# Kernel optimization log

Measured on AMD Instinct MI355X. Metric: run time of the kernel, lower is better.

## Reference

```python
import jax, jax.numpy as jnp
import numpy as np

N_HEADS = 16
EPS = 1e-12  # torch F.normalize eps


def srmsnorm(x):
    # F.normalize(x, dim=-1) * sqrt(dim)
    d = x.shape[-1]
    norm = jnp.sqrt(jnp.sum(x * x, axis=-1, keepdims=True))
    return x / jnp.maximum(norm, EPS) * jnp.sqrt(jnp.float32(d))


def setup_inputs() -> dict:
    key = jax.random.key(0)
    ks = jax.random.split(key, 7)
    B, S, D, F = 2, 2048, 1024, 4096
    x = jax.random.normal(ks[0], (B, S, D), dtype=jnp.float32)
    # xavier-uniform-ish scale for square weights
    lim = np.sqrt(6.0 / (D + D)).astype(np.float32)
    wq = jax.random.uniform(ks[1], (D, D), jnp.float32, -lim, lim)
    wk = jax.random.uniform(ks[2], (D, D), jnp.float32, -lim, lim)
    wv = jax.random.uniform(ks[3], (D, D), jnp.float32, -lim, lim)
    wo = jax.random.uniform(ks[4], (D, D), jnp.float32, -lim, lim)
    w_in = jax.random.normal(ks[5], (D, F), dtype=jnp.float32) * np.sqrt(2.0 / D).astype(np.float32)
    lim2 = np.sqrt(6.0 / (D + F)).astype(np.float32)
    w_out = jax.random.uniform(ks[6], (F, D), jnp.float32, -lim2, lim2)
    return {"x": x, "wq": wq, "wk": wk, "wv": wv, "wo": wo, "w_in": w_in, "w_out": w_out}


def attention(x, wq, wk, wv, wo):
    B, S, D = x.shape
    H = N_HEADS
    hd = D // H
    scale = hd ** -0.5
    q = (x @ wq).reshape(B, S, H, hd).transpose(0, 2, 1, 3)  # [B,H,S,hd]
    k = (x @ wk).reshape(B, S, H, hd).transpose(0, 2, 1, 3)
    v = (x @ wv).reshape(B, S, H, hd).transpose(0, 2, 1, 3)
    scores = jnp.einsum('bhqd,bhkd->bhqk', q, k) * scale  # [B,H,S,S]
    causal = jnp.tril(jnp.ones((S, S), dtype=bool))
    scores = jnp.where(causal, scores, jnp.float32(-jnp.inf))
    probs = jax.nn.softmax(scores, axis=-1)
    out = jnp.einsum('bhqk,bhkd->bhqd', probs, v)  # [B,H,S,hd]
    out = out.transpose(0, 2, 1, 3).reshape(B, S, D)
    return out @ wo


def reference(x, wq, wk, wv, wo, w_in, w_out):
    h = x + attention(srmsnorm(x), wq, wk, wv, wo)
    ff = jax.nn.gelu(srmsnorm(h) @ w_in, approximate=True) @ w_out
    return h + ff
```

## Files before the change

kernel.cpp:

```cpp
#include <hip/hip_runtime.h>
#include <math.h>

#define BB 2
#define SS 2048
#define DD 1024
#define FF 4096
#define HH 16
#define MM (BB * SS)

typedef __attribute__((ext_vector_type(8))) short short8v;
typedef __attribute__((ext_vector_type(4))) float float4v;
typedef __attribute__((ext_vector_type(4))) unsigned short ushort4v;
typedef __attribute__((ext_vector_type(8))) unsigned short ushort8v;
typedef unsigned short u16;
typedef unsigned int u32;

#define MFMA16(A_, B_, C_) __builtin_amdgcn_mfma_f32_16x16x32_bf16((A_), (B_), (C_), 0, 0, 0)

__device__ __forceinline__ u16 f2bf(float f) {
    u32 u = __float_as_uint(f);
    u += 0x7FFF + ((u >> 16) & 1);
    return (u16)(u >> 16);
}

__device__ __forceinline__ void async16(void* lds, const void* g) {
    __builtin_amdgcn_global_load_lds(
        (const __attribute__((address_space(1))) u32*)g,
        (__attribute__((address_space(3))) u32*)lds, 16, 0, 0);
}

__device__ __forceinline__ float gelu_f(float x) {
    float u = 0.7978845608028654f * x * (1.0f + 0.044715f * x * x);
    float e = exp2f(u * 2.8853900817779268f);
    float th = 1.0f - 2.0f / (e + 1.0f);
    return 0.5f * x * (1.0f + th);
}

__global__ __launch_bounds__(256) void srmsnorm_bf16(const float* __restrict__ in,
                                                     u16* __restrict__ out) {
    const int row = blockIdx.x, t = threadIdx.x;
    float4 a = reinterpret_cast<const float4*>(in + (size_t)row * DD)[t];
    float ss = a.x * a.x + a.y * a.y + a.z * a.z + a.w * a.w;
#pragma unroll
    for (int off = 32; off > 0; off >>= 1) ss += __shfl_xor(ss, off);
    __shared__ float red[4];
    if ((t & 63) == 0) red[t >> 6] = ss;
    __syncthreads();
    float tot = red[0] + red[1] + red[2] + red[3];
    float sc = 32.0f / fmaxf(sqrtf(tot), 1e-12f);
    ushort4v ov;
    ov[0] = f2bf(a.x * sc); ov[1] = f2bf(a.y * sc);
    ov[2] = f2bf(a.z * sc); ov[3] = f2bf(a.w * sc);
    *(ushort4v*)(out + (size_t)row * DD + t * 4) = ov;
}

__global__ __launch_bounds__(256) void wtrans(const float* __restrict__ in,
                                              u16* __restrict__ out, int K, int N) {
    __shared__ float T[64][65];
    const int t = threadIdx.x;
    const int n0 = blockIdx.x * 64, k0 = blockIdx.y * 64;
#pragma unroll
    for (int i = 0; i < 4; ++i) {
        int r = i * 16 + (t >> 4), c4 = (t & 15) * 4;
        float4 v = *reinterpret_cast<const float4*>(in + (size_t)(k0 + r) * N + n0 + c4);
        T[r][c4 + 0] = v.x; T[r][c4 + 1] = v.y; T[r][c4 + 2] = v.z; T[r][c4 + 3] = v.w;
    }
    __syncthreads();
#pragma unroll
    for (int i = 0; i < 4; ++i) {
        int r = i * 16 + (t >> 4), c4 = (t & 15) * 4;
        ushort4v ov;
#pragma unroll
        for (int j = 0; j < 4; ++j) ov[j] = f2bf(T[c4 + j][r]);
        *(ushort4v*)(out + (size_t)(n0 + r) * K + k0 + c4) = ov;
    }
}

__global__ __launch_bounds__(256) void vtrans(const u16* __restrict__ vb,
                                              u16* __restrict__ vt) {
    __shared__ u16 T[64][88];
    const int t = threadIdx.x;
    const int s0 = blockIdx.x * 64, bh = blockIdx.y;
    const int b = bh >> 4, h = bh & 15;
#pragma unroll
    for (int i = 0; i < 2; ++i) {
        int r = i * 32 + (t >> 3), c8 = (t & 7) * 8;
        *(ushort8v*)&T[r][c8] =
            *(const ushort8v*)(vb + (size_t)(b * SS + s0 + r) * DD + h * 64 + c8);
    }
    __syncthreads();
#pragma unroll
    for (int i = 0; i < 2; ++i) {
        int d = i * 32 + (t >> 3), s8 = (t & 7) * 8;
        ushort8v ov;
#pragma unroll
        for (int j = 0; j < 8; ++j) ov[j] = T[s8 + j][d];
        *(ushort8v*)(vt + ((size_t)bh * 64 + d) * SS + s0 + s8) = ov;
    }
}

template <int BM, int BN, int EPI>
__global__ __launch_bounds__(256) void gemm_bf16(const u16* __restrict__ A,
                                                 const u16* __restrict__ Bt,
                                                 const float* __restrict__ Res,
                                                 void* __restrict__ Cout,
                                                 int M, int N, int K) {
    __shared__ u16 As[BM * 32];
    __shared__ u16 Bs[BN * 32];
    constexpr int FM = BM / 32, FN = BN / 32;
    const int t = threadIdx.x;
    const int w = t >> 6, lane = t & 63;
    const int g = lane >> 4, c = lane & 15;
    const int wr = w >> 1, wc = w & 1;
    const int bm = blockIdx.y * BM, bn = blockIdx.x * BN;
    const int arow = t >> 2, au = (t & 3) * 8;

    float4v acc[FM][FN] = {};
    for (int k0 = 0; k0 < K; k0 += 32) {
        __syncthreads();
#pragma unroll
        for (int p = 0; p < BM / 64; ++p)
            async16(&As[(p * 64 + arow) * 32 + au],
                    A + (size_t)(bm + p * 64 + arow) * K + k0 + au);
#pragma unroll
        for (int p = 0; p < BN / 64; ++p)
            async16(&Bs[(p * 64 + arow) * 32 + au],
                    Bt + (size_t)(bn + p * 64 + arow) * K + k0 + au);
        __syncthreads();
        short8v af[FM], bf[FN];
#pragma unroll
        for (int mi = 0; mi < FM; ++mi)
            af[mi] = *(const short8v*)&As[(wr * (BM / 2) + mi * 16 + c) * 32 + g * 8];
#pragma unroll
        for (int ni = 0; ni < FN; ++ni)
            bf[ni] = *(const short8v*)&Bs[(wc * (BN / 2) + ni * 16 + c) * 32 + g * 8];
#pragma unroll
        for (int mi = 0; mi < FM; ++mi)
#pragma unroll
            for (int ni = 0; ni < FN; ++ni)
                acc[mi][ni] = MFMA16(af[mi], bf[ni], acc[mi][ni]);
    }
    const int row0 = bm + wr * (BM / 2), col0 = bn + wc * (BN / 2);
#pragma unroll
    for (int mi = 0; mi < FM; ++mi)
#pragma unroll
        for (int r = 0; r < 4; ++r) {
            const size_t rw = (size_t)(row0 + mi * 16 + 4 * g + r) * N;
#pragma unroll
            for (int ni = 0; ni < FN; ++ni) {
                const size_t off = rw + col0 + ni * 16 + c;
                float v = acc[mi][ni][r];
                if (EPI == 0)      ((u16*)Cout)[off] = f2bf(v);
                else if (EPI == 1) ((float*)Cout)[off] = v + Res[off];
                else               ((u16*)Cout)[off] = f2bf(gelu_f(v));
            }
        }
}

__global__ __launch_bounds__(256) void attn_mfma(const u16* __restrict__ Qb,
                                                 const u16* __restrict__ Kb,
                                                 const u16* __restrict__ Vt,
                                                 u16* __restrict__ Ao) {
    __shared__ u16 Pl[4][2][16][88];
    const int t = threadIdx.x;
    const int w = t >> 6, lane = t & 63;
    const int g = lane >> 4, c = lane & 15;
    const int bh = blockIdx.x;
    const int qt = (int)(gridDim.y - 1) - (int)blockIdx.y;
    const int b = bh >> 4, h = bh & 15;
    const int qrow0 = qt * 128 + w * 32;
    const int ktmax = (qrow0 + 31) >> 6;
    const size_t qkbase = (size_t)b * SS * DD + h * 64;
    const size_t vbase = (size_t)bh * 64 * SS;
    constexpr float SC = 0.18033688011112042f;

    short8v qf[2][2];
#pragma unroll
    for (int rb = 0; rb < 2; ++rb)
#pragma unroll
        for (int kh = 0; kh < 2; ++kh)
            qf[rb][kh] = *(const short8v*)(Qb + qkbase +
                             (size_t)(qrow0 + rb * 16 + c) * DD + kh * 32 + g * 8);

    float4v o[2][4] = {};
    float m_run[2][4], l_run[2][4];
#pragma unroll
    for (int rb = 0; rb < 2; ++rb)
#pragma unroll
        for (int r = 0; r < 4; ++r) { m_run[rb][r] = -1e30f; l_run[rb][r] = 0.0f; }

    for (int kt = 0; kt <= ktmax; ++kt) {
        short8v kf[4][2];
#pragma unroll
        for (int nb = 0; nb < 4; ++nb)
#pragma unroll
            for (int kh = 0; kh < 2; ++kh)
                kf[nb][kh] = *(const short8v*)(Kb + qkbase +
                                 (size_t)(kt * 64 + nb * 16 + c) * DD + kh * 32 + g * 8);
        float4v sa[2][4] = {};
#pragma unroll
        for (int nb = 0; nb < 4; ++nb)
#pragma unroll
            for (int kh = 0; kh < 2; ++kh)
#pragma unroll
                for (int rb = 0; rb < 2; ++rb)
                    sa[rb][nb] = MFMA16(qf[rb][kh], kf[nb][kh], sa[rb][nb]);

        const bool diag = (kt == ktmax);
#pragma unroll
        for (int rb = 0; rb < 2; ++rb)
#pragma unroll
            for (int nb = 0; nb < 4; ++nb)
#pragma unroll
                for (int r = 0; r < 4; ++r) {
                    float v = sa[rb][nb][r] * SC;
                    if (diag && (kt * 64 + nb * 16 + c > qrow0 + rb * 16 + 4 * g + r))
                        v = -3e38f;
                    sa[rb][nb][r] = v;
                }

#pragma unroll
        for (int rb = 0; rb < 2; ++rb) {
            float mx[4], corr[4];
#pragma unroll
            for (int r = 0; r < 4; ++r) {
                float m0 = fmaxf(fmaxf(sa[rb][0][r], sa[rb][1][r]),
                                 fmaxf(sa[rb][2][r], sa[rb][3][r]));
                m0 = fmaxf(m0, __shfl_xor(m0, 1));
                m0 = fmaxf(m0, __shfl_xor(m0, 2));
                m0 = fmaxf(m0, __shfl_xor(m0, 4));
                m0 = fmaxf(m0, __shfl_xor(m0, 8));
                float mn = fmaxf(m_run[rb][r], m0);
                corr[r] = exp2f(m_run[rb][r] - mn);
                m_run[rb][r] = mn;
                mx[r] = mn;
            }
#pragma unroll
            for (int nb = 0; nb < 4; ++nb)
#pragma unroll
                for (int r = 0; r < 4; ++r)
                    sa[rb][nb][r] = exp2f(sa[rb][nb][r] - mx[r]);
#pragma unroll
            for (int r = 0; r < 4; ++r) {
                float s_ = sa[rb][0][r] + sa[rb][1][r] + sa[rb][2][r] + sa[rb][3][r];
                s_ += __shfl_xor(s_, 1); s_ += __shfl_xor(s_, 2);
                s_ += __shfl_xor(s_, 4); s_ += __shfl_xor(s_, 8);
                l_run[rb][r] = l_run[rb][r] * corr[r] + s_;
            }
            float4v cv; cv[0] = corr[0]; cv[1] = corr[1]; cv[2] = corr[2]; cv[3] = corr[3];
#pragma unroll
            for (int nb = 0; nb < 4; ++nb) o[rb][nb] *= cv;
#pragma unroll
            for (int nb = 0; nb < 4; ++nb)
#pragma unroll
                for (int r = 0; r < 4; ++r)
                    Pl[w][rb][4 * g + r][nb * 16 + c] = f2bf(sa[rb][nb][r]);
        }

        short8v pa[2][2];
#pragma unroll
        for (int rb = 0; rb < 2; ++rb)
#pragma unroll
            for (int kh = 0; kh < 2; ++kh)
                pa[rb][kh] = *(const short8v*)&Pl[w][rb][c][kh * 32 + g * 8];
        short8v vf[4][2];
#pragma unroll
        for (int nb = 0; nb < 4; ++nb)
#pragma unroll
            for (int kh = 0; kh < 2; ++kh)
                vf[nb][kh] = *(const short8v*)(Vt + vbase +
                                 (size_t)(nb * 16 + c) * SS + kt * 64 + kh * 32 + g * 8);
#pragma unroll
        for (int nb = 0; nb < 4; ++nb)
#pragma unroll
            for (int kh = 0; kh < 2; ++kh)
#pragma unroll
                for (int rb = 0; rb < 2; ++rb)
                    o[rb][nb] = MFMA16(pa[rb][kh], vf[nb][kh], o[rb][nb]);
    }

#pragma unroll
    for (int rb = 0; rb < 2; ++rb) {
        float inv[4];
#pragma unroll
        for (int r = 0; r < 4; ++r) inv[r] = 1.0f / l_run[rb][r];
#pragma unroll
        for (int nb = 0; nb < 4; ++nb)
#pragma unroll
            for (int r = 0; r < 4; ++r)
                Ao[qkbase + (size_t)(qrow0 + rb * 16 + 4 * g + r) * DD + nb * 16 + c] =
                    f2bf(o[rb][nb][r] * inv[r]);
    }
}

extern "C" void kernel_launch(void* const* d_in, const int* in_sizes, int n_in,
                              void* d_out, int out_size, void* d_ws, size_t ws_size,
                              hipStream_t stream) {
    const float* x     = (const float*)d_in[0];
    const float* wq    = (const float*)d_in[1];
    const float* wk    = (const float*)d_in[2];
    const float* wv    = (const float*)d_in[3];
    const float* wo    = (const float*)d_in[4];
    const float* w_in  = (const float*)d_in[5];
    const float* w_out = (const float*)d_in[6];
    float* out = (float*)d_out;
    char* ws = (char*)d_ws;
    const size_t MB = 1024 * 1024;
    u16* wq_t  = (u16*)(ws + 0 * MB);
    u16* wk_t  = (u16*)(ws + 2 * MB);
    u16* wv_t  = (u16*)(ws + 4 * MB);
    u16* wo_t  = (u16*)(ws + 6 * MB);
    u16* wi_t  = (u16*)(ws + 8 * MB);
    u16* wo2_t = (u16*)(ws + 16 * MB);
    u16* xn    = (u16*)(ws + 24 * MB);
    u16* qb    = (u16*)(ws + 32 * MB);
    u16* kb    = (u16*)(ws + 40 * MB);
    u16* vb    = (u16*)(ws + 48 * MB);
    u16* vt    = (u16*)(ws + 56 * MB);
    u16* ao    = (u16*)(ws + 64 * MB);
    u16* hn    = (u16*)(ws + 72 * MB);
    u16* gbuf  = (u16*)(ws + 80 * MB);

    dim3 blk(256);
    wtrans<<<dim3(DD / 64, DD / 64), blk, 0, stream>>>(wq, wq_t, DD, DD);
    wtrans<<<dim3(DD / 64, DD / 64), blk, 0, stream>>>(wk, wk_t, DD, DD);
    wtrans<<<dim3(DD / 64, DD / 64), blk, 0, stream>>>(wv, wv_t, DD, DD);
    wtrans<<<dim3(DD / 64, DD / 64), blk, 0, stream>>>(wo, wo_t, DD, DD);
    wtrans<<<dim3(FF / 64, DD / 64), blk, 0, stream>>>(w_in, wi_t, DD, FF);
    wtrans<<<dim3(DD / 64, FF / 64), blk, 0, stream>>>(w_out, wo2_t, FF, DD);

    srmsnorm_bf16<<<MM, blk, 0, stream>>>(x, xn);
    gemm_bf16<128, 64, 0><<<dim3(DD / 64, MM / 128), blk, 0, stream>>>(xn, wq_t, nullptr, qb, MM, DD, DD);
    gemm_bf16<128, 64, 0><<<dim3(DD / 64, MM / 128), blk, 0, stream>>>(xn, wk_t, nullptr, kb, MM, DD, DD);
    gemm_bf16<128, 64, 0><<<dim3(DD / 64, MM / 128), blk, 0, stream>>>(xn, wv_t, nullptr, vb, MM, DD, DD);
    vtrans<<<dim3(SS / 64, BB * HH), blk, 0, stream>>>(vb, vt);
    attn_mfma<<<dim3(BB * HH, SS / 128), blk, 0, stream>>>(qb, kb, vt, ao);
    gemm_bf16<128, 64, 1><<<dim3(DD / 64, MM / 128), blk, 0, stream>>>(ao, wo_t, x, out, MM, DD, DD);
    srmsnorm_bf16<<<MM, blk, 0, stream>>>(out, hn);
    gemm_bf16<128, 128, 2><<<dim3(FF / 128, MM / 128), blk, 0, stream>>>(hn, wi_t, nullptr, gbuf, MM, FF, DD);
    gemm_bf16<128, 64, 1><<<dim3(DD / 64, MM / 128), blk, 0, stream>>>(gbuf, wo2_t, out, out, MM, DD, FF);
}
```

Measured before the change: 459.4 us.

## Fuse weight transposes and QKV GEMMs, split attention into single-wave blocks

```diff
diff --git a/kernel.cpp b/kernel.cpp
--- a/kernel.cpp
+++ b/kernel.cpp
@@ -54,11 +54,9 @@
     *(ushort4v*)(out + (size_t)row * DD + t * 4) = ov;
 }
 
-__global__ __launch_bounds__(256) void wtrans(const float* __restrict__ in,
-                                              u16* __restrict__ out, int K, int N) {
-    __shared__ float T[64][65];
-    const int t = threadIdx.x;
-    const int n0 = blockIdx.x * 64, k0 = blockIdx.y * 64;
+__device__ __forceinline__ void trans_tile(const float* __restrict__ in,
+                                           u16* __restrict__ out, int K, int N,
+                                           int n0, int k0, int t, float (*T)[65]) {
 #pragma unroll
     for (int i = 0; i < 4; ++i) {
         int r = i * 16 + (t >> 4), c4 = (t & 15) * 4;
@@ -73,6 +71,33 @@
 #pragma unroll
         for (int j = 0; j < 4; ++j) ov[j] = f2bf(T[c4 + j][r]);
         *(ushort4v*)(out + (size_t)(n0 + r) * K + k0 + c4) = ov;
+    }
+}
+
+__global__ __launch_bounds__(256) void wtrans_all(const float* __restrict__ wq,
+                                                  const float* __restrict__ wk,
+                                                  const float* __restrict__ wv,
+                                                  const float* __restrict__ wo,
+                                                  const float* __restrict__ wi,
+                                                  const float* __restrict__ wo2,
+                                                  char* __restrict__ ws) {
+    __shared__ float T[64][65];
+    const int t = threadIdx.x;
+    const size_t MB = 1024 * 1024;
+    int id = blockIdx.x;
+    if (id < 1024) {
+        const int which = id >> 8, l = id & 255;
+        const float* in = which == 0 ? wq : which == 1 ? wk : which == 2 ? wv : wo;
+        u16* out = (u16*)(ws + (size_t)which * 2 * MB);
+        trans_tile(in, out, 1024, 1024, (l & 15) * 64, (l >> 4) * 64, t, T);
+    } else if (id < 2048) {
+        const int l = id - 1024;
+        trans_tile(wi, (u16*)(ws + 8 * MB), 1024, 4096,
+                   (l & 63) * 64, (l >> 6) * 64, t, T);
+    } else {
+        const int l = id - 2048;
+        trans_tile(wo2, (u16*)(ws + 16 * MB), 4096, 1024,
+                   (l & 15) * 64, (l >> 4) * 64, t, T);
     }
 }
 
@@ -141,6 +166,20 @@
                 acc[mi][ni] = MFMA16(af[mi], bf[ni], acc[mi][ni]);
     }
     const int row0 = bm + wr * (BM / 2), col0 = bn + wc * (BN / 2);
+    if (EPI == 3) {
+        const int seg = col0 >> 10, c0 = col0 & 1023;
+        u16* dst = (u16*)Cout + (size_t)seg * ((size_t)MM * 1024);
+#pragma unroll
+        for (int mi = 0; mi < FM; ++mi)
+#pragma unroll
+            for (int r = 0; r < 4; ++r) {
+                const size_t rw = (size_t)(row0 + mi * 16 + 4 * g + r) * 1024;
+#pragma unroll
+                for (int ni = 0; ni < FN; ++ni)
+                    dst[rw + c0 + ni * 16 + c] = f2bf(acc[mi][ni][r]);
+            }
+        return;
+    }
 #pragma unroll
     for (int mi = 0; mi < FM; ++mi)
 #pragma unroll
@@ -157,19 +196,19 @@
         }
 }
 
-__global__ __launch_bounds__(256) void attn_mfma(const u16* __restrict__ Qb,
-                                                 const u16* __restrict__ Kb,
-                                                 const u16* __restrict__ Vt,
-                                                 u16* __restrict__ Ao) {
-    __shared__ u16 Pl[4][2][16][88];
-    const int t = threadIdx.x;
-    const int w = t >> 6, lane = t & 63;
+__global__ __launch_bounds__(64) void attn_mfma(const u16* __restrict__ Qb,
+                                                const u16* __restrict__ Kb,
+                                                const u16* __restrict__ Vt,
+                                                u16* __restrict__ Ao) {
+    __shared__ u16 Pl[2][16][88];
+    const int lane = threadIdx.x;
     const int g = lane >> 4, c = lane & 15;
-    const int bh = blockIdx.x;
-    const int qt = (int)(gridDim.y - 1) - (int)blockIdx.y;
+    const int bid = blockIdx.x;
+    const int bh = bid & 31;
+    const int u = 63 - (bid >> 5);
     const int b = bh >> 4, h = bh & 15;
-    const int qrow0 = qt * 128 + w * 32;
-    const int ktmax = (qrow0 + 31) >> 6;
+    const int qrow0 = u * 32;
+    const int ktmax = qrow0 >> 6;
     const size_t qkbase = (size_t)b * SS * DD + h * 64;
     const size_t vbase = (size_t)bh * 64 * SS;
     constexpr float SC = 0.18033688011112042f;
@@ -198,6 +237,7 @@
                 kf[nb][kh] = *(const short8v*)(Kb + qkbase +
                                  (size_t)(kt * 64 + nb * 16 + c) * DD + kh * 32 + g * 8);
         float4v sa[2][4] = {};
+        __builtin_amdgcn_s_setprio(1);
 #pragma unroll
         for (int nb = 0; nb < 4; ++nb)
 #pragma unroll
@@ -205,6 +245,7 @@
 #pragma unroll
                 for (int rb = 0; rb < 2; ++rb)
                     sa[rb][nb] = MFMA16(qf[rb][kh], kf[nb][kh], sa[rb][nb]);
+        __builtin_amdgcn_s_setprio(0);
 
         const bool diag = (kt == ktmax);
 #pragma unroll
@@ -221,7 +262,7 @@
 
 #pragma unroll
         for (int rb = 0; rb < 2; ++rb) {
-            float mx[4], corr[4];
+            float corr[4];
 #pragma unroll
             for (int r = 0; r < 4; ++r) {
                 float m0 = fmaxf(fmaxf(sa[rb][0][r], sa[rb][1][r]),
@@ -233,13 +274,12 @@
                 float mn = fmaxf(m_run[rb][r], m0);
                 corr[r] = exp2f(m_run[rb][r] - mn);
                 m_run[rb][r] = mn;
-                mx[r] = mn;
             }
 #pragma unroll
             for (int nb = 0; nb < 4; ++nb)
 #pragma unroll
                 for (int r = 0; r < 4; ++r)
-                    sa[rb][nb][r] = exp2f(sa[rb][nb][r] - mx[r]);
+                    sa[rb][nb][r] = exp2f(sa[rb][nb][r] - m_run[rb][r]);
 #pragma unroll
             for (int r = 0; r < 4; ++r) {
                 float s_ = sa[rb][0][r] + sa[rb][1][r] + sa[rb][2][r] + sa[rb][3][r];
@@ -254,7 +294,7 @@
             for (int nb = 0; nb < 4; ++nb)
 #pragma unroll
                 for (int r = 0; r < 4; ++r)
-                    Pl[w][rb][4 * g + r][nb * 16 + c] = f2bf(sa[rb][nb][r]);
+                    Pl[rb][4 * g + r][nb * 16 + c] = f2bf(sa[rb][nb][r]);
         }
 
         short8v pa[2][2];
@@ -262,7 +302,7 @@
         for (int rb = 0; rb < 2; ++rb)
 #pragma unroll
             for (int kh = 0; kh < 2; ++kh)
-                pa[rb][kh] = *(const short8v*)&Pl[w][rb][c][kh * 32 + g * 8];
+                pa[rb][kh] = *(const short8v*)&Pl[rb][c][kh * 32 + g * 8];
         short8v vf[4][2];
 #pragma unroll
         for (int nb = 0; nb < 4; ++nb)
@@ -270,6 +310,7 @@
             for (int kh = 0; kh < 2; ++kh)
                 vf[nb][kh] = *(const short8v*)(Vt + vbase +
                                  (size_t)(nb * 16 + c) * SS + kt * 64 + kh * 32 + g * 8);
+        __builtin_amdgcn_s_setprio(1);
 #pragma unroll
         for (int nb = 0; nb < 4; ++nb)
 #pragma unroll
@@ -277,6 +318,7 @@
 #pragma unroll
                 for (int rb = 0; rb < 2; ++rb)
                     o[rb][nb] = MFMA16(pa[rb][kh], vf[nb][kh], o[rb][nb]);
+        __builtin_amdgcn_s_setprio(0);
     }
 
 #pragma unroll
@@ -307,14 +349,11 @@
     char* ws = (char*)d_ws;
     const size_t MB = 1024 * 1024;
     u16* wq_t  = (u16*)(ws + 0 * MB);
-    u16* wk_t  = (u16*)(ws + 2 * MB);
-    u16* wv_t  = (u16*)(ws + 4 * MB);
     u16* wo_t  = (u16*)(ws + 6 * MB);
     u16* wi_t  = (u16*)(ws + 8 * MB);
     u16* wo2_t = (u16*)(ws + 16 * MB);
     u16* xn    = (u16*)(ws + 24 * MB);
     u16* qb    = (u16*)(ws + 32 * MB);
-    u16* kb    = (u16*)(ws + 40 * MB);
     u16* vb    = (u16*)(ws + 48 * MB);
     u16* vt    = (u16*)(ws + 56 * MB);
     u16* ao    = (u16*)(ws + 64 * MB);
@@ -322,21 +361,15 @@
     u16* gbuf  = (u16*)(ws + 80 * MB);
 
     dim3 blk(256);
-    wtrans<<<dim3(DD / 64, DD / 64), blk, 0, stream>>>(wq, wq_t, DD, DD);
-    wtrans<<<dim3(DD / 64, DD / 64), blk, 0, stream>>>(wk, wk_t, DD, DD);
-    wtrans<<<dim3(DD / 64, DD / 64), blk, 0, stream>>>(wv, wv_t, DD, DD);
-    wtrans<<<dim3(DD / 64, DD / 64), blk, 0, stream>>>(wo, wo_t, DD, DD);
-    wtrans<<<dim3(FF / 64, DD / 64), blk, 0, stream>>>(w_in, wi_t, DD, FF);
-    wtrans<<<dim3(DD / 64, FF / 64), blk, 0, stream>>>(w_out, wo2_t, FF, DD);
+    wtrans_all<<<dim3(3072), blk, 0, stream>>>(wq, wk, wv, wo, w_in, w_out, ws);
 
     srmsnorm_bf16<<<MM, blk, 0, stream>>>(x, xn);
-    gemm_bf16<128, 64, 0><<<dim3(DD / 64, MM / 128), blk, 0, stream>>>(xn, wq_t, nullptr, qb, MM, DD, DD);
-    gemm_bf16<128, 64, 0><<<dim3(DD / 64, MM / 128), blk, 0, stream>>>(xn, wk_t, nullptr, kb, MM, DD, DD);
-    gemm_bf16<128, 64, 0><<<dim3(DD / 64, MM / 128), blk, 0, stream>>>(xn, wv_t, nullptr, vb, MM, DD, DD);
+    gemm_bf16<128, 128, 3><<<dim3(3072 / 128, MM / 128), blk, 0, stream>>>(
+        xn, wq_t, nullptr, qb, MM, 3072, DD);
     vtrans<<<dim3(SS / 64, BB * HH), blk, 0, stream>>>(vb, vt);
-    attn_mfma<<<dim3(BB * HH, SS / 128), blk, 0, stream>>>(qb, kb, vt, ao);
-    gemm_bf16<128, 64, 1><<<dim3(DD / 64, MM / 128), blk, 0, stream>>>(ao, wo_t, x, out, MM, DD, DD);
+    attn_mfma<<<dim3(32 * 64), dim3(64), 0, stream>>>(qb, qb + (size_t)MM * 1024, vt, ao);
+    gemm_bf16<128, 128, 1><<<dim3(DD / 128, MM / 128), blk, 0, stream>>>(ao, wo_t, x, out, MM, DD, DD);
     srmsnorm_bf16<<<MM, blk, 0, stream>>>(out, hn);
     gemm_bf16<128, 128, 2><<<dim3(FF / 128, MM / 128), blk, 0, stream>>>(hn, wi_t, nullptr, gbuf, MM, FF, DD);
-    gemm_bf16<128, 64, 1><<<dim3(DD / 64, MM / 128), blk, 0, stream>>>(gbuf, wo2_t, out, out, MM, DD, FF);
-}
+    gemm_bf16<128, 128, 1><<<dim3(DD / 128, MM / 128), blk, 0, stream>>>(gbuf, wo2_t, out, out, MM, DD, FF);
+}
```

Measured after the change: 430.2 us. 1.07x faster.
